# Performance work log

Hardware: AMD Instinct MI355X
Metric: run time of the kernel (lower is better)

The kernel has to match this reference:

```python
import jax, jax.numpy as jnp
import numpy as np
import math

KEY_SIZE = 128  # init arg; scale = 1/sqrt(key_size)


def setup_inputs() -> dict:
    key = jax.random.key(0)
    kq, kk, kv = jax.random.split(key, 3)
    B, LQ, LK, D, DV = 16, 2048, 2048, 128, 128
    q = jax.random.normal(kq, (B, LQ, D), dtype=jnp.float32)
    k = jax.random.normal(kk, (B, LK, D), dtype=jnp.float32)
    v = jax.random.normal(kv, (B, LK, DV), dtype=jnp.float32)
    return {"q": q, "k": k, "v": v}


def reference(q, k, v):
    scale = 1.0 / math.sqrt(KEY_SIZE)
    # scores: [B, Lq, Lk]
    scores = jnp.einsum('bqd,bkd->bqk', q, k) * scale
    probs = jax.nn.softmax(scores, axis=-1)
    # dropout with p=0.0 is identity (eval-equivalent)
    return jnp.einsum('bqk,bkv->bqv', probs, v)
```

## Files before the change

kernel.cpp:

```cpp
#include <hip/hip_runtime.h>
#include <hip/hip_bf16.h>

typedef float f32x4 __attribute__((ext_vector_type(4)));
typedef float f32x16 __attribute__((ext_vector_type(16)));
typedef short bf16x8 __attribute__((ext_vector_type(8)));
typedef unsigned u32x4 __attribute__((ext_vector_type(4)));

constexpr int NB = 16, LQ = 2048, LK = 2048, D = 128, DV = 128;
constexpr int KVBLK = 64;
constexpr int NTH = 16;
constexpr float SCALE = 0.08838834764831843f;
constexpr float LOG2E = 1.4426950408889634f;
constexpr float QSCALE = SCALE * LOG2E;

__device__ __forceinline__ unsigned short f2bfs(float f) {
  __hip_bfloat16 h = __float2bfloat16(f);
  return __builtin_bit_cast(unsigned short, h);
}

__device__ __forceinline__ unsigned short f2bf(float f) {
  unsigned int u = __float_as_uint(f);
  u += 0x7FFFu + ((u >> 16) & 1u);
  return (unsigned short)(u >> 16);
}

__device__ __forceinline__ int swz2(int row) {
  return (row ^ (row >> 1) ^ (row >> 3)) & 7;
}

__device__ __forceinline__ int swap23(int m) {
  return (m & ~12) | ((m & 4) << 1) | ((m & 8) >> 1);
}

typedef const __attribute__((address_space(1))) void* gas1_t;
typedef __attribute__((address_space(3))) void* las3_t;
__device__ __forceinline__ void gload16(const void* g, void* l) {
  __builtin_amdgcn_global_load_lds((gas1_t)g, (las3_t)l, 16, 0, 0);
}

__device__ __forceinline__ unsigned pk2(float lo, float hi) {
  unsigned short a = f2bfs(lo), b = f2bfs(hi);
  return (unsigned)a | ((unsigned)b << 16);
}

__device__ __forceinline__ void mk_pb(const f32x16& s, bf16x8& pe, bf16x8& po) {
  u32x4 e = {pk2(s[0], s[1]), pk2(s[2], s[3]), pk2(s[4], s[5]), pk2(s[6], s[7])};
  pe = __builtin_bit_cast(bf16x8, e);
  u32x4 od = {pk2(s[8], s[9]), pk2(s[10], s[11]), pk2(s[12], s[13]), pk2(s[14], s[15])};
  po = __builtin_bit_cast(bf16x8, od);
}

__global__ __launch_bounds__(256) void conv_bf16(const float* __restrict__ in,
                                                 unsigned short* __restrict__ out,
                                                 float scale) {
  int i = blockIdx.x * 256 + threadIdx.x;
  f32x4 a = ((const f32x4*)in)[2 * i];
  f32x4 b = ((const f32x4*)in)[2 * i + 1];
  bf16x8 r;
  #pragma unroll
  for (int j = 0; j < 4; ++j) {
    r[j]     = (short)f2bfs(a[j] * scale);
    r[4 + j] = (short)f2bfs(b[j] * scale);
  }
  ((bf16x8*)out)[i] = r;
}

__global__ __launch_bounds__(256) void conv_vt(const float* __restrict__ v,
                                               unsigned short* __restrict__ vt) {
  __shared__ __align__(16) unsigned short tb[64 * 64];
  const int tid = threadIdx.x;
  const int k0 = blockIdx.x * 64, dv0 = blockIdx.y * 64, b = blockIdx.z;
  {
    const int kk = tid >> 2, dd0 = (tid & 3) * 16;
    const float* src = v + ((long)(b * LK + k0 + kk)) * DV + dv0 + dd0;
    f32x4 a0 = ((const f32x4*)src)[0];
    f32x4 a1 = ((const f32x4*)src)[1];
    f32x4 a2 = ((const f32x4*)src)[2];
    f32x4 a3 = ((const f32x4*)src)[3];
    bf16x8 r0, r1;
    #pragma unroll
    for (int j = 0; j < 4; ++j) {
      r0[j] = (short)f2bfs(a0[j]); r0[4 + j] = (short)f2bfs(a1[j]);
      r1[j] = (short)f2bfs(a2[j]); r1[4 + j] = (short)f2bfs(a3[j]);
    }
    int ch = dd0 >> 3;
    *(bf16x8*)&tb[kk * 64 + ((ch ^ swz2(kk)) << 3)] = r0;
    *(bf16x8*)&tb[kk * 64 + (((ch + 1) ^ swz2(kk)) << 3)] = r1;
  }
  __syncthreads();
  {
    const int dv = tid >> 2, ks = (tid & 3) * 16;
    bf16x8 w0, w1;
    #pragma unroll
    for (int j = 0; j < 8; ++j) {
      int r0 = ks + j, r1 = ks + 8 + j;
      w0[j] = (short)tb[r0 * 64 + (((dv >> 3) ^ swz2(r0)) << 3) + (dv & 7)];
      w1[j] = (short)tb[r1 * 64 + (((dv >> 3) ^ swz2(r1)) << 3) + (dv & 7)];
    }
    unsigned short* dst = vt + ((long)(b * DV + dv0 + dv)) * LK + k0 + ks;
    *(bf16x8*)dst = w0;
    *(bf16x8*)(dst + 8) = w1;
  }
}

__global__ __launch_bounds__(512, 2) void attn_fwd5(
    const float* __restrict__ qp, const unsigned short* __restrict__ wsK,
    const unsigned short* __restrict__ wsVt, float* __restrict__ op) {
  __shared__ __align__(16) unsigned short sm[65536];

  const int tid = threadIdx.x;
  const int wid = tid >> 6;
  const int h2  = wid >> 2;
  const int lane = tid & 63;
  const int q32 = lane & 31;
  const int hi  = lane >> 5;
  const int ht  = tid & 255;

  const int bid = blockIdx.x;
  const int sbid = (bid & 7) * 32 + (bid >> 3);
  const int b = sbid >> 4;
  const int qb = (sbid & 15) * 128;
  const int qwave = qb + (wid & 3) * 32;

  bf16x8 aq[8];
  {
    const float* qrow = qp + ((long)(b * LQ + qwave + q32)) * D + hi * 8;
    #pragma unroll
    for (int st = 0; st < 8; ++st) {
      f32x4 x0 = *(const f32x4*)(qrow + st * 16);
      f32x4 x1 = *(const f32x4*)(qrow + st * 16 + 4);
      #pragma unroll
      for (int j = 0; j < 4; ++j) {
        aq[st][j]     = (short)f2bfs(x0[j] * QSCALE);
        aq[st][4 + j] = (short)f2bfs(x1[j] * QSCALE);
      }
    }
  }
  __builtin_amdgcn_sched_barrier(0);

  const unsigned short* kbatch = wsK + (long)b * LK * D;
  const unsigned short* vbatch = wsVt + (long)b * DV * LK;
  const int kvbase = h2 * 1024;
  const int lbase = h2 * 32768;

  const unsigned short* ksp[4];
  const unsigned short* vsp[4];
  unsigned ldk[4], ldv[4];
  #pragma unroll
  for (int it = 0; it < 4; ++it) {
    int ci = it * 256 + ht;
    int krow = ci >> 4, kc16 = ci & 15;
    ksp[it] = kbatch + (long)kvbase * D + swap23(krow) * D +
              ((kc16 ^ swz2(krow)) << 3);
    ldk[it] = lbase + ci * 8;
    int vrow = ci >> 3, vc8 = ci & 7;
    vsp[it] = vbatch + (long)vrow * LK + kvbase + ((vc8 ^ swz2(vrow)) << 3);
    ldv[it] = lbase + 8192 + ci * 8;
  }

  auto stage = [&](int buf, int t) {
    const int ko = t * (KVBLK * D);
    const int vo = t * KVBLK;
    const int lb = buf * 16384;
    #pragma unroll
    for (int it = 0; it < 4; ++it)
      gload16(ksp[it] + ko, &sm[ldk[it] + lb]);
    #pragma unroll
    for (int it = 0; it < 4; ++it)
      gload16(vsp[it] + vo, &sm[ldv[it] + lb]);
  };

  stage(0, 0);
  stage(1, 1);

  f32x16 o[4];
  #pragma unroll
  for (int mt = 0; mt < 4; ++mt) o[mt] = (f32x16){};
  float m_s = -1e30f, l_s = 0.f;

  for (int t = 0; t < NTH; ++t) {
    if (t < NTH - 1) {
      asm volatile("s_waitcnt vmcnt(8)" ::: "memory");
    } else {
      asm volatile("s_waitcnt vmcnt(0)" ::: "memory");
    }
    __builtin_amdgcn_sched_barrier(0);
    __builtin_amdgcn_s_barrier();
    __builtin_amdgcn_sched_barrier(0);

    const int cur = t & 1;
    const int kb = lbase + cur * 16384, vb = kb + 8192;

    f32x16 s0 = (f32x16){}, s1 = (f32x16){};
    __builtin_amdgcn_s_setprio(1);
    #pragma unroll
    for (int st = 0; st < 8; ++st) {
      const int c16 = 2 * st + hi;
      const int r0 = q32;
      bf16x8 k0 = *(const bf16x8*)&sm[kb + r0 * 128 + ((c16 ^ swz2(r0)) << 3)];
      s0 = __builtin_amdgcn_mfma_f32_32x32x16_bf16(k0, aq[st], s0, 0, 0, 0);
      const int r1 = 32 + q32;
      bf16x8 k1 = *(const bf16x8*)&sm[kb + r1 * 128 + ((c16 ^ swz2(r1)) << 3)];
      s1 = __builtin_amdgcn_mfma_f32_32x32x16_bf16(k1, aq[st], s1, 0, 0, 0);
    }
    __builtin_amdgcn_s_setprio(0);

    float pm = s0[0];
    #pragma unroll
    for (int i = 1; i < 16; ++i) pm = fmaxf(pm, s0[i]);
    #pragma unroll
    for (int i = 0; i < 16; ++i) pm = fmaxf(pm, s1[i]);
    pm = fmaxf(pm, __shfl_xor(pm, 32));
    if (!__all(pm <= m_s + 8.0f)) {
      float mn = fmaxf(m_s, pm);
      float al = exp2f(m_s - mn);
      l_s *= al;
      #pragma unroll
      for (int mt = 0; mt < 4; ++mt)
        #pragma unroll
        for (int i = 0; i < 16; ++i) o[mt][i] *= al;
      m_s = mn;
    }
    float sum = 0.f;
    #pragma unroll
    for (int i = 0; i < 16; ++i) { s0[i] = exp2f(s0[i] - m_s); sum += s0[i]; }
    #pragma unroll
    for (int i = 0; i < 16; ++i) { s1[i] = exp2f(s1[i] - m_s); sum += s1[i]; }
    l_s += sum + __shfl_xor(sum, 32);

    bf16x8 pb[4];
    mk_pb(s0, pb[0], pb[1]);
    mk_pb(s1, pb[2], pb[3]);

    __builtin_amdgcn_s_setprio(1);
    #pragma unroll
    for (int ks = 0; ks < 4; ++ks) {
      const int c8 = 2 * ks + hi;
      #pragma unroll
      for (int mt = 0; mt < 4; ++mt) {
        const int row = mt * 32 + q32;
        bf16x8 vf = *(const bf16x8*)&sm[vb + row * 64 + ((c8 ^ swz2(row)) << 3)];
        o[mt] = __builtin_amdgcn_mfma_f32_32x32x16_bf16(vf, pb[ks], o[mt], 0, 0, 0);
      }
    }
    __builtin_amdgcn_s_setprio(0);

    __builtin_amdgcn_sched_barrier(0);
    __builtin_amdgcn_s_barrier();
    __builtin_amdgcn_sched_barrier(0);

    if (t < NTH - 2) stage(cur, t + 2);
  }

  float* scr = (float*)sm;
  float* wreg = scr + (size_t)(wid & 3) * 4352;
  __syncthreads();
  if (h2 == 1) {
    #pragma unroll
    for (int j4 = 0; j4 < 16; ++j4) {
      const int mt = j4 >> 2, a = j4 & 3;
      f32x4 v = {o[mt][4 * a], o[mt][4 * a + 1], o[mt][4 * a + 2], o[mt][4 * a + 3]};
      *(f32x4*)&wreg[lane * 64 + ((j4 ^ (lane & 15)) << 2)] = v;
    }
    wreg[4096 + lane * 2] = m_s;
    wreg[4096 + lane * 2 + 1] = l_s;
  }
  __syncthreads();
  if (h2 == 0) {
    const float m1 = wreg[4096 + lane * 2];
    const float l1 = wreg[4096 + lane * 2 + 1];
    const float mm = fmaxf(m_s, m1);
    float a0 = exp2f(m_s - mm), a1 = exp2f(m1 - mm);
    const float inv = 1.f / (a0 * l_s + a1 * l1);
    a0 *= inv;
    a1 *= inv;
    float* dst = op + ((long)(b * LQ + qwave + q32)) * DV;
    #pragma unroll
    for (int j4 = 0; j4 < 16; ++j4) {
      const int mt = j4 >> 2, a = j4 & 3;
      f32x4 pv = *(const f32x4*)&wreg[lane * 64 + ((j4 ^ (lane & 15)) << 2)];
      f32x4 r;
      #pragma unroll
      for (int i = 0; i < 4; ++i) r[i] = a0 * o[mt][4 * a + i] + a1 * pv[i];
      *(f32x4*)&dst[32 * mt + 8 * a + 4 * hi] = r;
    }
  }
}

__device__ __forceinline__ int swzc(int row, int c16) {
  return c16 ^ ((row ^ (row >> 3)) & 7);
}

__global__ __launch_bounds__(256, 2) void attn_fwd(
    const float* __restrict__ qp, const float* __restrict__ kp,
    const float* __restrict__ vp, float* __restrict__ op) {
  __shared__ __align__(16) unsigned short smm[28672];
  const int tid = threadIdx.x, wid = tid >> 6, lane = tid & 63;
  const int g = lane >> 4, c = lane & 15;
  const int b = blockIdx.y, qb = blockIdx.x * 64;
  const float* qg = qp + ((long)b * LQ + qb) * D;
  const float* kg = kp + (long)b * LK * D;
  const float* vg = vp + (long)b * LK * DV;
  #pragma unroll
  for (int it = 0; it < 4; ++it) {
    int ch = it * 256 + tid, row = ch >> 4, c16 = ch & 15;
    const float* src = qg + row * D + c16 * 8;
    f32x4 f0 = *(const f32x4*)(src);
    f32x4 f1 = *(const f32x4*)(src + 4);
    bf16x8 fr;
    #pragma unroll
    for (int j = 0; j < 4; ++j) {
      fr[j] = (short)f2bf(f0[j] * SCALE);
      fr[4 + j] = (short)f2bf(f1[j] * SCALE);
    }
    *(bf16x8*)&smm[row * 128 + swzc(row, c16) * 8] = fr;
  }
  __syncthreads();
  bf16x8 aq[4];
  #pragma unroll
  for (int ks = 0; ks < 4; ++ks) {
    int row = wid * 16 + c;
    aq[ks] = *(const bf16x8*)&smm[row * 128 + swzc(row, ks * 4 + g) * 8];
  }
  f32x4 o[8]; f32x4 fz = {0.f, 0.f, 0.f, 0.f};
  #pragma unroll
  for (int i = 0; i < 8; ++i) o[i] = fz;
  float m_r[4] = {-1e30f, -1e30f, -1e30f, -1e30f};
  float l_r[4] = {0.f, 0.f, 0.f, 0.f};
  const int pbase = 24576 + wid * 1024;
  for (int kv0 = 0; kv0 < LK; kv0 += KVBLK) {
    __syncthreads();
    const float* ksrc = kg + (long)kv0 * D;
    #pragma unroll
    for (int it = 0; it < 4; ++it) {
      int ch = it * 256 + tid, row = ch >> 4, c16 = ch & 15;
      const float* src = ksrc + row * D + c16 * 8;
      f32x4 f0 = *(const f32x4*)(src);
      f32x4 f1 = *(const f32x4*)(src + 4);
      bf16x8 fr;
      #pragma unroll
      for (int j = 0; j < 4; ++j) { fr[j] = (short)f2bf(f0[j]); fr[4 + j] = (short)f2bf(f1[j]); }
      *(bf16x8*)&smm[8192 + row * 128 + swzc(row, c16) * 8] = fr;
    }
    {
      const float* vsrc = vg + (long)kv0 * DV;
      int dvq = (tid & 31) * 4, kg8 = tid >> 5;
      f32x4 col[8];
      #pragma unroll
      for (int j = 0; j < 8; ++j) col[j] = *(const f32x4*)(vsrc + (kg8 * 8 + j) * DV + dvq);
      #pragma unroll
      for (int i = 0; i < 4; ++i) {
        int dv = dvq + i;
        bf16x8 fr;
        #pragma unroll
        for (int j = 0; j < 8; ++j) fr[j] = (short)f2bf(col[j][i]);
        *(bf16x8*)&smm[16384 + dv * 64 + swzc(dv, kg8) * 8] = fr;
      }
    }
    __syncthreads();
    f32x4 s[4];
    #pragma unroll
    for (int i = 0; i < 4; ++i) s[i] = fz;
    #pragma unroll
    for (int ks = 0; ks < 4; ++ks) {
      #pragma unroll
      for (int t = 0; t < 4; ++t) {
        int row = t * 16 + c;
        bf16x8 bk = *(const bf16x8*)&smm[8192 + row * 128 + swzc(row, ks * 4 + g) * 8];
        s[t] = __builtin_amdgcn_mfma_f32_16x16x32_bf16(aq[ks], bk, s[t], 0, 0, 0);
      }
    }
    #pragma unroll
    for (int r = 0; r < 4; ++r) {
      float pm = fmaxf(fmaxf(s[0][r], s[1][r]), fmaxf(s[2][r], s[3][r]));
      pm = fmaxf(pm, __shfl_xor(pm, 1));
      pm = fmaxf(pm, __shfl_xor(pm, 2));
      pm = fmaxf(pm, __shfl_xor(pm, 4));
      pm = fmaxf(pm, __shfl_xor(pm, 8));
      float mn = fmaxf(m_r[r], pm);
      float al = exp2f((m_r[r] - mn) * LOG2E);
      float sum = 0.f;
      #pragma unroll
      for (int t = 0; t < 4; ++t) {
        float p = exp2f((s[t][r] - mn) * LOG2E);
        s[t][r] = p; sum += p;
      }
      sum += __shfl_xor(sum, 1); sum += __shfl_xor(sum, 2);
      sum += __shfl_xor(sum, 4); sum += __shfl_xor(sum, 8);
      l_r[r] = l_r[r] * al + sum; m_r[r] = mn;
      #pragma unroll
      for (int dvt = 0; dvt < 8; ++dvt) o[dvt][r] *= al;
    }
    #pragma unroll
    for (int t = 0; t < 4; ++t)
      #pragma unroll
      for (int r = 0; r < 4; ++r) {
        int row = g * 4 + r, colx = c + 16 * t;
        smm[pbase + row * 64 + swzc(row, colx >> 3) * 8 + (colx & 7)] = f2bf(s[t][r]);
      }
    #pragma unroll
    for (int ks = 0; ks < 2; ++ks) {
      bf16x8 pa = *(const bf16x8*)&smm[pbase + c * 64 + swzc(c, ks * 4 + g) * 8];
      #pragma unroll
      for (int dvt = 0; dvt < 8; ++dvt) {
        int row = dvt * 16 + c;
        bf16x8 vb2 = *(const bf16x8*)&smm[16384 + row * 64 + swzc(row, ks * 4 + g) * 8];
        o[dvt] = __builtin_amdgcn_mfma_f32_16x16x32_bf16(pa, vb2, o[dvt], 0, 0, 0);
      }
    }
  }
  float* dst = op + ((long)b * LQ + qb + wid * 16) * DV;
  #pragma unroll
  for (int r = 0; r < 4; ++r) {
    float inv = 1.f / l_r[r];
    #pragma unroll
    for (int dvt = 0; dvt < 8; ++dvt)
      dst[(g * 4 + r) * DV + dvt * 16 + c] = o[dvt][r] * inv;
  }
}

extern "C" void kernel_launch(void* const* d_in, const int* in_sizes, int n_in,
                              void* d_out, int out_size, void* d_ws, size_t ws_size,
                              hipStream_t stream) {
  const float* q = (const float*)d_in[0];
  const float* k = (const float*)d_in[1];
  const float* v = (const float*)d_in[2];
  float* out = (float*)d_out;

  const size_t kelems = (size_t)NB * LK * D;
  const size_t need = kelems * 2 * 2;
  if (ws_size >= need) {
    unsigned short* wsK = (unsigned short*)d_ws;
    unsigned short* wsVt = wsK + kelems;
    conv_bf16<<<dim3((int)(kelems / 8 / 256)), dim3(256), 0, stream>>>(k, wsK, 1.0f);
    conv_vt<<<dim3(LK / 64, DV / 64, NB), dim3(256), 0, stream>>>(v, wsVt);
    attn_fwd5<<<dim3(NB * LQ / 128), dim3(512), 0, stream>>>(q, wsK, wsVt, out);
  } else {
    attn_fwd<<<dim3(LQ / 64, NB), dim3(256), 0, stream>>>(q, k, v, out);
  }
}
```

Baseline: 75.55 us.

## Shrink attention tiles to 64 query rows and 32-key KV blocks

Reworks the fused attention kernel to use 256-thread blocks covering 64 query rows, with 32-key KV tiles. The grid doubles to 512 blocks and shared memory is halved. The V tile now uses a new swizzled layout, and V fragments are loaded from LDS before the softmax so the reads overlap the exp work. Each K-V sweep still splits the key range across two wave halves. The aim is better occupancy and load balance across CUs, at the cost of twice as many loop iterations and barriers and less K/V reuse per block. The max and sum reductions also become trees instead of linear chains.

```diff
diff --git a/kernel.cpp b/kernel.cpp
--- a/kernel.cpp
+++ b/kernel.cpp
@@ -7,8 +7,8 @@
 typedef unsigned u32x4 __attribute__((ext_vector_type(4)));
 
 constexpr int NB = 16, LQ = 2048, LK = 2048, D = 128, DV = 128;
-constexpr int KVBLK = 64;
-constexpr int NTH = 16;
+constexpr int KVBLK = 32;
+constexpr int NTH = 32;
 constexpr float SCALE = 0.08838834764831843f;
 constexpr float LOG2E = 1.4426950408889634f;
 constexpr float QSCALE = SCALE * LOG2E;
@@ -103,24 +103,24 @@
   }
 }
 
-__global__ __launch_bounds__(512, 2) void attn_fwd5(
+__global__ __launch_bounds__(256, 2) void attn_fwd6(
     const float* __restrict__ qp, const unsigned short* __restrict__ wsK,
     const unsigned short* __restrict__ wsVt, float* __restrict__ op) {
-  __shared__ __align__(16) unsigned short sm[65536];
+  __shared__ __align__(16) unsigned short sm[32768];
 
   const int tid = threadIdx.x;
   const int wid = tid >> 6;
-  const int h2  = wid >> 2;
+  const int h2  = wid >> 1;
   const int lane = tid & 63;
   const int q32 = lane & 31;
   const int hi  = lane >> 5;
-  const int ht  = tid & 255;
+  const int ht  = tid & 127;
 
   const int bid = blockIdx.x;
-  const int sbid = (bid & 7) * 32 + (bid >> 3);
-  const int b = sbid >> 4;
-  const int qb = (sbid & 15) * 128;
-  const int qwave = qb + (wid & 3) * 32;
+  const int sbid = (bid & 7) * 64 + (bid >> 3);
+  const int b = sbid >> 5;
+  const int qb = (sbid & 31) * 64;
+  const int qwave = qb + (wid & 1) * 32;
 
   bf16x8 aq[8];
   {
@@ -141,33 +141,33 @@
   const unsigned short* kbatch = wsK + (long)b * LK * D;
   const unsigned short* vbatch = wsVt + (long)b * DV * LK;
   const int kvbase = h2 * 1024;
-  const int lbase = h2 * 32768;
+  const int lbase = h2 * 16384;
 
   const unsigned short* ksp[4];
   const unsigned short* vsp[4];
   unsigned ldk[4], ldv[4];
   #pragma unroll
   for (int it = 0; it < 4; ++it) {
-    int ci = it * 256 + ht;
+    int ci = it * 128 + ht;
     int krow = ci >> 4, kc16 = ci & 15;
-    ksp[it] = kbatch + (long)kvbase * D + swap23(krow) * D +
+    ksp[it] = kbatch + ((long)kvbase + swap23(krow)) * D +
               ((kc16 ^ swz2(krow)) << 3);
     ldk[it] = lbase + ci * 8;
-    int vrow = ci >> 3, vc8 = ci & 7;
-    vsp[it] = vbatch + (long)vrow * LK + kvbase + ((vc8 ^ swz2(vrow)) << 3);
-    ldv[it] = lbase + 8192 + ci * 8;
+    int r64 = ci >> 3, ch = ci & 7;
+    int L = ch ^ swz2(r64);
+    int dv = 2 * r64 + (L >> 2), kc = L & 3;
+    vsp[it] = vbatch + (long)dv * LK + kvbase + kc * 8;
+    ldv[it] = lbase + 4096 + ci * 8;
   }
 
   auto stage = [&](int buf, int t) {
-    const int ko = t * (KVBLK * D);
-    const int vo = t * KVBLK;
-    const int lb = buf * 16384;
+    const int lb = buf * 8192;
     #pragma unroll
     for (int it = 0; it < 4; ++it)
-      gload16(ksp[it] + ko, &sm[ldk[it] + lb]);
+      gload16(ksp[it] + t * (KVBLK * D), &sm[ldk[it] + lb]);
     #pragma unroll
     for (int it = 0; it < 4; ++it)
-      gload16(vsp[it] + vo, &sm[ldv[it] + lb]);
+      gload16(vsp[it] + t * KVBLK, &sm[ldv[it] + lb]);
   };
 
   stage(0, 0);
@@ -189,27 +189,36 @@
     __builtin_amdgcn_sched_barrier(0);
 
     const int cur = t & 1;
-    const int kb = lbase + cur * 16384, vb = kb + 8192;
-
-    f32x16 s0 = (f32x16){}, s1 = (f32x16){};
+    const int kb = lbase + cur * 8192, vb = kb + 4096;
+
+    f32x16 s0 = (f32x16){};
     __builtin_amdgcn_s_setprio(1);
     #pragma unroll
     for (int st = 0; st < 8; ++st) {
       const int c16 = 2 * st + hi;
-      const int r0 = q32;
-      bf16x8 k0 = *(const bf16x8*)&sm[kb + r0 * 128 + ((c16 ^ swz2(r0)) << 3)];
+      bf16x8 k0 = *(const bf16x8*)&sm[kb + q32 * 128 + ((c16 ^ swz2(q32)) << 3)];
       s0 = __builtin_amdgcn_mfma_f32_32x32x16_bf16(k0, aq[st], s0, 0, 0, 0);
-      const int r1 = 32 + q32;
-      bf16x8 k1 = *(const bf16x8*)&sm[kb + r1 * 128 + ((c16 ^ swz2(r1)) << 3)];
-      s1 = __builtin_amdgcn_mfma_f32_32x32x16_bf16(k1, aq[st], s1, 0, 0, 0);
     }
     __builtin_amdgcn_s_setprio(0);
 
-    float pm = s0[0];
-    #pragma unroll
-    for (int i = 1; i < 16; ++i) pm = fmaxf(pm, s0[i]);
-    #pragma unroll
-    for (int i = 0; i < 16; ++i) pm = fmaxf(pm, s1[i]);
+    bf16x8 vf[8];
+    #pragma unroll
+    for (int ks = 0; ks < 2; ++ks) {
+      #pragma unroll
+      for (int mt = 0; mt < 4; ++mt) {
+        const int row = mt * 32 + q32;
+        const int r64 = row >> 1;
+        const int L = (row & 1) * 4 + 2 * ks + hi;
+        vf[ks * 4 + mt] = *(const bf16x8*)&sm[vb + r64 * 64 + ((L ^ swz2(r64)) << 3)];
+      }
+    }
+
+    float m8[8];
+    #pragma unroll
+    for (int i = 0; i < 8; ++i) m8[i] = fmaxf(s0[i], s0[i + 8]);
+    float m4a = fmaxf(m8[0], m8[1]), m4b = fmaxf(m8[2], m8[3]);
+    float m4c = fmaxf(m8[4], m8[5]), m4d = fmaxf(m8[6], m8[7]);
+    float pm = fmaxf(fmaxf(m4a, m4b), fmaxf(m4c, m4d));
     pm = fmaxf(pm, __shfl_xor(pm, 32));
     if (!__all(pm <= m_s + 8.0f)) {
       float mn = fmaxf(m_s, pm);
@@ -221,28 +230,26 @@
         for (int i = 0; i < 16; ++i) o[mt][i] *= al;
       m_s = mn;
     }
-    float sum = 0.f;
-    #pragma unroll
-    for (int i = 0; i < 16; ++i) { s0[i] = exp2f(s0[i] - m_s); sum += s0[i]; }
-    #pragma unroll
-    for (int i = 0; i < 16; ++i) { s1[i] = exp2f(s1[i] - m_s); sum += s1[i]; }
+    #pragma unroll
+    for (int i = 0; i < 16; ++i) s0[i] = exp2f(s0[i] - m_s);
+    float s8[8];
+    #pragma unroll
+    for (int i = 0; i < 8; ++i) s8[i] = s0[i] + s0[i + 8];
+    float s4a = (s8[0] + s8[1]) + (s8[2] + s8[3]);
+    float s4b = (s8[4] + s8[5]) + (s8[6] + s8[7]);
+    float sum = s4a + s4b;
     l_s += sum + __shfl_xor(sum, 32);
 
-    bf16x8 pb[4];
-    mk_pb(s0, pb[0], pb[1]);
-    mk_pb(s1, pb[2], pb[3]);
+    bf16x8 pb0, pb1;
+    mk_pb(s0, pb0, pb1);
 
     __builtin_amdgcn_s_setprio(1);
     #pragma unroll
-    for (int ks = 0; ks < 4; ++ks) {
-      const int c8 = 2 * ks + hi;
-      #pragma unroll
-      for (int mt = 0; mt < 4; ++mt) {
-        const int row = mt * 32 + q32;
-        bf16x8 vf = *(const bf16x8*)&sm[vb + row * 64 + ((c8 ^ swz2(row)) << 3)];
-        o[mt] = __builtin_amdgcn_mfma_f32_32x32x16_bf16(vf, pb[ks], o[mt], 0, 0, 0);
-      }
-    }
+    for (int mt = 0; mt < 4; ++mt)
+      o[mt] = __builtin_amdgcn_mfma_f32_32x32x16_bf16(vf[mt], pb0, o[mt], 0, 0, 0);
+    #pragma unroll
+    for (int mt = 0; mt < 4; ++mt)
+      o[mt] = __builtin_amdgcn_mfma_f32_32x32x16_bf16(vf[4 + mt], pb1, o[mt], 0, 0, 0);
     __builtin_amdgcn_s_setprio(0);
 
     __builtin_amdgcn_sched_barrier(0);
@@ -253,7 +260,7 @@
   }
 
   float* scr = (float*)sm;
-  float* wreg = scr + (size_t)(wid & 3) * 4352;
+  float* wreg = scr + (size_t)(wid & 1) * 4352;
   __syncthreads();
   if (h2 == 1) {
     #pragma unroll
@@ -328,7 +335,7 @@
   float m_r[4] = {-1e30f, -1e30f, -1e30f, -1e30f};
   float l_r[4] = {0.f, 0.f, 0.f, 0.f};
   const int pbase = 24576 + wid * 1024;
-  for (int kv0 = 0; kv0 < LK; kv0 += KVBLK) {
+  for (int kv0 = 0; kv0 < LK; kv0 += 64) {
     __syncthreads();
     const float* ksrc = kg + (long)kv0 * D;
     #pragma unroll
@@ -434,7 +441,7 @@
     unsigned short* wsVt = wsK + kelems;
     conv_bf16<<<dim3((int)(kelems / 8 / 256)), dim3(256), 0, stream>>>(k, wsK, 1.0f);
     conv_vt<<<dim3(LK / 64, DV / 64, NB), dim3(256), 0, stream>>>(v, wsVt);
-    attn_fwd5<<<dim3(NB * LQ / 128), dim3(512), 0, stream>>>(q, wsK, wsVt, out);
+    attn_fwd6<<<dim3(NB * LQ / 64), dim3(256), 0, stream>>>(q, wsK, wsVt, out);
   } else {
     attn_fwd<<<dim3(LQ / 64, NB), dim3(256), 0, stream>>>(q, k, v, out);
   }
```

Result: slower. 79.43 us (+5.1%).
